# Kernel optimization log

Measured on AMD Instinct MI355X. Metric: run time of the kernel, lower is better.

## Reference

```python
import jax, jax.numpy as jnp
import numpy as np

NHEADS = 16
LORA_SCALE = 16.0 / 16.0  # alpha / r


def lora_linear(x, W, b, A, B):
    # base projection + low-rank LoRA path: x@W^T + b + s*(x@A^T)@B^T
    base = jnp.einsum('bse,oe->bso', x, W) + b
    low = jnp.einsum('bse,re->bsr', x, A)  # [B,S,r]
    return base + LORA_SCALE * jnp.einsum('bsr,or->bso', low, B)


def setup_inputs() -> dict:
    key = jax.random.key(0)
    E, R = 1024, 16
    ks = jax.random.split(key, 20)
    d = {'x': jax.random.normal(ks[0], (4, 1024, E), jnp.float32)}
    i = 1
    for p in ('q', 'k', 'v', 'o'):
        d[f'{p}_w'] = jax.random.normal(ks[i], (E, E), jnp.float32) * 0.02; i += 1
        d[f'{p}_b'] = jax.random.normal(ks[i], (E,), jnp.float32) * 0.02; i += 1
        d[f'{p}_la'] = jax.random.normal(ks[i], (R, E), jnp.float32) * 0.02; i += 1
        d[f'{p}_lb'] = jax.random.normal(ks[i], (E, R), jnp.float32) * 0.02; i += 1
    return d


def reference(x, q_w, q_b, q_la, q_lb, k_w, k_b, k_la, k_lb,
              v_w, v_b, v_la, v_lb, o_w, o_b, o_la, o_lb):
    B, S, E = x.shape
    H = NHEADS
    D = E // H
    q = lora_linear(x, q_w, q_b, q_la, q_lb).reshape(B, S, H, D)
    k = lora_linear(x, k_w, k_b, k_la, k_lb).reshape(B, S, H, D)
    v = lora_linear(x, v_w, v_b, v_la, v_lb).reshape(B, S, H, D)
    scores = jnp.einsum('bshd,bthd->bhst', q, k) / jnp.sqrt(jnp.asarray(D, x.dtype))
    attn = jax.nn.softmax(scores, axis=-1)
    ctx = jnp.einsum('bhst,bthd->bshd', attn, v).reshape(B, S, E)
    return lora_linear(ctx, o_w, o_b, o_la, o_lb)
```

## Files before the change

kernel.cpp:

```cpp
#include <hip/hip_runtime.h>
#include <cstdint>


typedef __attribute__((ext_vector_type(8))) short bf16x8;
typedef __attribute__((ext_vector_type(4))) float f32x4;
typedef __attribute__((ext_vector_type(16))) float f32x16;
typedef __attribute__((ext_vector_type(4))) unsigned short u16x4;
typedef __attribute__((ext_vector_type(4))) unsigned int u32x4;

__device__ __forceinline__ short f2bf(float f) {
  unsigned u = __builtin_bit_cast(unsigned, f);
  u += 0x7FFFu + ((u >> 16) & 1u);
  return (short)(u >> 16);
}

typedef __attribute__((address_space(1))) const unsigned int as1_uint;
typedef __attribute__((address_space(3))) unsigned int as3_uint;

__device__ __forceinline__ void gload_lds16(const short* g, const short* l) {
  __builtin_amdgcn_global_load_lds((as1_uint*)g,
      (as3_uint*)(unsigned int)(uintptr_t)l, 16, 0, 0);
}

__device__ __forceinline__ unsigned cvtpk(float lo, float hi) {
  unsigned r;
  asm("v_cvt_pk_bf16_f32 %0, %1, %2" : "=v"(r) : "v"(lo), "v"(hi));
  return r;
}
__device__ __forceinline__ void plswap(unsigned &a, unsigned &b) {
  asm("v_permlane32_swap_b32 %0, %1" : "+v"(a), "+v"(b));
}

__device__ __forceinline__ void build_pfrag(const f32x16 &s, bf16x8 &f0, bf16x8 &f1) {
  unsigned x0 = cvtpk(s[0], s[1]),  x1 = cvtpk(s[2], s[3]);
  unsigned x2 = cvtpk(s[4], s[5]),  x3 = cvtpk(s[6], s[7]);
  plswap(x0, x2); plswap(x1, x3);
  unsigned y0 = cvtpk(s[8], s[9]),  y1 = cvtpk(s[10], s[11]);
  unsigned y2 = cvtpk(s[12], s[13]), y3 = cvtpk(s[14], s[15]);
  plswap(y0, y2); plswap(y1, y3);
  u32x4 a = {x0, x1, x2, x3}, b = {y0, y1, y2, y3};
  f0 = __builtin_bit_cast(bf16x8, a);
  f1 = __builtin_bit_cast(bf16x8, b);
}

__global__ void build_x(const float* __restrict__ x, short* __restrict__ xb) {
  int idx = blockIdx.x * 256 + threadIdx.x;
  f32x4 v = ((const f32x4*)x)[idx];
  u16x4 o;
  o[0] = (unsigned short)f2bf(v[0]);
  o[1] = (unsigned short)f2bf(v[1]);
  o[2] = (unsigned short)f2bf(v[2]);
  o[3] = (unsigned short)f2bf(v[3]);
  ((u16x4*)xb)[idx] = o;
}

__global__ void fold_w(const float* __restrict__ wq, const float* __restrict__ wk,
                       const float* __restrict__ wv, const float* __restrict__ wo,
                       const float* __restrict__ bq, const float* __restrict__ bk,
                       const float* __restrict__ bv, const float* __restrict__ bo,
                       const float* __restrict__ aq, const float* __restrict__ ak,
                       const float* __restrict__ av, const float* __restrict__ ao,
                       short* __restrict__ out) {
  const int p = blockIdx.y;
  const float* W  = (p == 0) ? wq : (p == 1) ? wk : (p == 2) ? wv : wo;
  const float* Bm = (p == 0) ? bq : (p == 1) ? bk : (p == 2) ? bv : bo;
  const float* A  = (p == 0) ? aq : (p == 1) ? ak : (p == 2) ? av : ao;
  const int idx = blockIdx.x * 256 + threadIdx.x;
  const int n = idx >> 8;
  const int e4 = idx & 255;
  f32x4 acc = ((const f32x4*)(W + (size_t)n * 1024))[e4];
  const float* br = Bm + n * 16;
  #pragma unroll
  for (int r = 0; r < 16; ++r) {
    const f32x4 a4 = ((const f32x4*)(A + (size_t)r * 1024))[e4];
    const float b = br[r];
    acc[0] += b * a4[0];
    acc[1] += b * a4[1];
    acc[2] += b * a4[2];
    acc[3] += b * a4[3];
  }
  u16x4 o;
  o[0] = (unsigned short)f2bf(acc[0]);
  o[1] = (unsigned short)f2bf(acc[1]);
  o[2] = (unsigned short)f2bf(acc[2]);
  o[3] = (unsigned short)f2bf(acc[3]);
  *(u16x4*)(out + (size_t)p * 1048576 + (size_t)idx * 4) = o;
}

__device__ __forceinline__ void gemm_core_p3(const short* __restrict__ xrow,
                                             const short* __restrict__ wrow,
                                             short (&As)[3][8192], short (&Bs)[3][8192],
                                             f32x4 (&acc)[4][4]) {
  const int tid = threadIdx.x;
  const int wv = tid >> 6, lane = tid & 63;
  const int wr = wv >> 1, wc = wv & 1;
  const int lrow = lane & 15, lk = lane >> 4;
  const int srow = lane >> 3, sphys = lane & 7;

#define STAGE_G(buf, kt)                                                       \
  {                                                                            \
    _Pragma("unroll")                                                          \
    for (int i = 0; i < 4; ++i) {                                              \
      const int ch = i * 4 + wv;                                               \
      const int row = ch * 8 + srow;                                           \
      const int sl = sphys ^ (row & 7);                                        \
      gload_lds16(xrow + (size_t)row * 1024 + (kt) * 64 + sl * 8, As[buf] + ch * 512); \
      gload_lds16(wrow + (size_t)row * 1024 + (kt) * 64 + sl * 8, Bs[buf] + ch * 512); \
    }                                                                          \
  }

  STAGE_G(0, 0);
  STAGE_G(1, 1);
  int cur = 0;
  for (int kt = 0; kt < 16; ++kt) {
    if (kt < 14) {
      const int nb = (cur == 0) ? 2 : (cur - 1);
      STAGE_G(nb, kt + 2);
      asm volatile("s_waitcnt vmcnt(16)" ::: "memory");
    } else if (kt == 14) {
      asm volatile("s_waitcnt vmcnt(8)" ::: "memory");
    } else {
      asm volatile("s_waitcnt vmcnt(0)" ::: "memory");
    }
    __builtin_amdgcn_s_barrier();

    #pragma unroll
    for (int kc = 0; kc < 2; ++kc) {
      bf16x8 af[4], bw[4];
      #pragma unroll
      for (int mi = 0; mi < 4; ++mi) {
        const int row = wr * 64 + mi * 16 + lrow;
        const int slot = (kc * 4 + lk) ^ (row & 7);
        af[mi] = *(const bf16x8*)(As[cur] + row * 64 + slot * 8);
      }
      #pragma unroll
      for (int nj = 0; nj < 4; ++nj) {
        const int row = wc * 64 + nj * 16 + lrow;
        const int slot = (kc * 4 + lk) ^ (row & 7);
        bw[nj] = *(const bf16x8*)(Bs[cur] + row * 64 + slot * 8);
      }
      #pragma unroll
      for (int mi = 0; mi < 4; ++mi)
        #pragma unroll
        for (int nj = 0; nj < 4; ++nj)
          acc[mi][nj] = __builtin_amdgcn_mfma_f32_16x16x32_bf16(af[mi], bw[nj], acc[mi][nj], 0, 0, 0);
    }

    asm volatile("s_waitcnt lgkmcnt(0)" ::: "memory");
    __builtin_amdgcn_s_barrier();
    cur = (cur == 2) ? 0 : (cur + 1);
  }
#undef STAGE_G
}

__global__ __launch_bounds__(256)
void gemm_qkv(const short* __restrict__ xb, const short* __restrict__ wb,
              const float* __restrict__ biasq, const float* __restrict__ biask,
              const float* __restrict__ biasv,
              short* __restrict__ qbuf, short* __restrict__ kbuf, short* __restrict__ vtb) {
  __shared__ short As[3][8192];
  __shared__ short Bs[3][8192];
  const int wg = blockIdx.x;
  const int xcd = wg & 7, ix = wg >> 3;
  const int bcol = xcd * 3 + ix % 3;
  const int brow = ix / 3;
  const int p = bcol >> 3;

  const f32x4 fz = {0.f, 0.f, 0.f, 0.f};
  f32x4 acc[4][4];
  #pragma unroll
  for (int a = 0; a < 4; ++a)
    #pragma unroll
    for (int b = 0; b < 4; ++b) acc[a][b] = fz;

  gemm_core_p3(xb + (size_t)brow * 128 * 1024,
               wb + (size_t)bcol * 128 * 1024, As, Bs, acc);

  const int tid = threadIdx.x;
  const int wv = tid >> 6, lane = tid & 63;
  const int wr = wv >> 1, wc = wv & 1;
  const int lrow = lane & 15, lk = lane >> 4;
  const float* bias = (p == 0) ? biasq : (p == 1) ? biask : biasv;
  const float oscale = (p == 0) ? 0.18033688f : 1.0f;
  const int c0 = (bcol & 7) * 128;
  float bcv[4];
  #pragma unroll
  for (int nj = 0; nj < 4; ++nj)
    bcv[nj] = bias[c0 + wc * 64 + nj * 16 + lrow];

  #pragma unroll
  for (int mi = 0; mi < 4; ++mi) {
    #pragma unroll
    for (int r = 0; r < 4; ++r) {
      const int gr = brow * 128 + wr * 64 + mi * 16 + lk * 4 + r;
      const int bb = gr >> 10, s = gr & 1023;
      #pragma unroll
      for (int nj = 0; nj < 4; ++nj) {
        const int gc = c0 + wc * 64 + nj * 16 + lrow;
        const float v = (acc[mi][nj][r] + bcv[nj]) * oscale;
        const int h = gc >> 6, d = gc & 63;
        const int bh = bb * 16 + h;
        if (p == 2)
          vtb[((size_t)bh * 64 + d) * 1024 + s] = f2bf(v);
        else
          ((p == 0) ? qbuf : kbuf)[((size_t)bh * 1024 + s) * 64 + d] = f2bf(v);
      }
    }
  }
}

__global__ __launch_bounds__(256)
void attn_kernel(const short* __restrict__ qbuf, const short* __restrict__ kbuf,
                 const short* __restrict__ vtb, short* __restrict__ cb) {
  __shared__ short Ks[2][64 * 64];
  __shared__ short Vs[2][64 * 64];
  const int bh = blockIdx.x, qt = blockIdx.y;
  const int tid = threadIdx.x, w = tid >> 6, lane = tid & 63;
  const int l31 = lane & 31, hi = lane >> 5;
  const int srow = lane >> 3, sphys = lane & 7;
  const short* Qp = qbuf + (size_t)bh * 65536;
  const short* Kp = kbuf + (size_t)bh * 65536;
  const short* Vp = vtb + (size_t)bh * 65536;
  const int q0 = qt * 128 + w * 32;

  bf16x8 bq[4];
  #pragma unroll
  for (int kc = 0; kc < 4; ++kc)
    bq[kc] = *(const bf16x8*)(Qp + (size_t)(q0 + l31) * 64 + kc * 16 + hi * 8);

  const f32x16 fz16 = {0.f,0.f,0.f,0.f,0.f,0.f,0.f,0.f,0.f,0.f,0.f,0.f,0.f,0.f,0.f,0.f};
  float m_run = -1e30f, l_run = 0.f;
  f32x16 acc0 = fz16, acc1 = fz16;

  #define STAGE_KV(buf, tt)                                                  \
    {                                                                        \
      const int t0s = (tt) * 64;                                             \
      _Pragma("unroll")                                                      \
      for (int i = 0; i < 2; ++i) {                                          \
        const int ch = i * 4 + w;                                            \
        const int row = ch * 8 + srow;                                       \
        const int sl = sphys ^ (row & 7);                                    \
        gload_lds16(Kp + (size_t)(t0s + row) * 64 + sl * 8, Ks[buf] + ch * 512); \
        gload_lds16(Vp + (size_t)row * 1024 + t0s + sl * 8, Vs[buf] + ch * 512); \
      }                                                                      \
    }

  STAGE_KV(0, 0);
  __syncthreads();

  int cur = 0;
  for (int tt = 0; tt < 16; ++tt) {
    if (tt < 15) STAGE_KV(cur ^ 1, tt + 1);

    f32x16 s0 = fz16, s1 = fz16;
    #pragma unroll
    for (int kc = 0; kc < 4; ++kc) {
      const int slot = (kc * 2 + hi) ^ (l31 & 7);
      const bf16x8 ak0 = *(const bf16x8*)(Ks[cur] + l31 * 64 + slot * 8);
      const bf16x8 ak1 = *(const bf16x8*)(Ks[cur] + (32 + l31) * 64 + slot * 8);
      s0 = __builtin_amdgcn_mfma_f32_32x32x16_bf16(ak0, bq[kc], s0, 0, 0, 0);
      s1 = __builtin_amdgcn_mfma_f32_32x32x16_bf16(ak1, bq[kc], s1, 0, 0, 0);
    }

    float tm = s0[0];
    #pragma unroll
    for (int r = 1; r < 16; ++r) tm = fmaxf(tm, s0[r]);
    #pragma unroll
    for (int r = 0; r < 16; ++r) tm = fmaxf(tm, s1[r]);
    tm = fmaxf(tm, __shfl_xor(tm, 32, 64));
    const float mn = fmaxf(m_run, tm);
    const float alpha = exp2f(m_run - mn);
    m_run = mn;
    float rs = 0.f;
    #pragma unroll
    for (int r = 0; r < 16; ++r) { const float p = exp2f(s0[r] - mn); s0[r] = p; rs += p; }
    #pragma unroll
    for (int r = 0; r < 16; ++r) { const float p = exp2f(s1[r] - mn); s1[r] = p; rs += p; }
    rs += __shfl_xor(rs, 32, 64);
    l_run = l_run * alpha + rs;
    #pragma unroll
    for (int r = 0; r < 16; ++r) { acc0[r] *= alpha; acc1[r] *= alpha; }

    bf16x8 pf[4];
    build_pfrag(s0, pf[0], pf[1]);
    build_pfrag(s1, pf[2], pf[3]);

    #pragma unroll
    for (int kc4 = 0; kc4 < 4; ++kc4) {
      const int slot = (kc4 * 2 + hi) ^ (l31 & 7);
      const bf16x8 av0 = *(const bf16x8*)(Vs[cur] + l31 * 64 + slot * 8);
      const bf16x8 av1 = *(const bf16x8*)(Vs[cur] + (32 + l31) * 64 + slot * 8);
      acc0 = __builtin_amdgcn_mfma_f32_32x32x16_bf16(av0, pf[kc4], acc0, 0, 0, 0);
      acc1 = __builtin_amdgcn_mfma_f32_32x32x16_bf16(av1, pf[kc4], acc1, 0, 0, 0);
    }

    __syncthreads();
    cur ^= 1;
  }

  const int bb = bh >> 4, h = bh & 15;
  const int s = q0 + l31;
  short* crow = cb + (size_t)(bb * 1024 + s) * 1024 + h * 64;
  const float inv = 1.f / l_run;
  #pragma unroll
  for (int rp = 0; rp < 8; ++rp) {
    const int r = rp * 2;
    const int d = (r & 3) + 8 * (r >> 2) + 4 * hi;
    const unsigned p0 = (unsigned)(unsigned short)f2bf(acc0[r] * inv)
                      | ((unsigned)(unsigned short)f2bf(acc0[r + 1] * inv) << 16);
    const unsigned p1 = (unsigned)(unsigned short)f2bf(acc1[r] * inv)
                      | ((unsigned)(unsigned short)f2bf(acc1[r + 1] * inv) << 16);
    *(unsigned*)(crow + d) = p0;
    *(unsigned*)(crow + 32 + d) = p1;
  }
  #undef STAGE_KV
}

__global__ __launch_bounds__(256)
void gemm_o(const short* __restrict__ cb, const short* __restrict__ wo,
            const float* __restrict__ biaso, float* __restrict__ out) {
  __shared__ short As[3][8192];
  __shared__ short Bs[3][8192];
  const int brow = blockIdx.y, bcol = blockIdx.x;
  const f32x4 fz = {0.f, 0.f, 0.f, 0.f};
  f32x4 acc[4][4];
  #pragma unroll
  for (int a = 0; a < 4; ++a)
    #pragma unroll
    for (int b = 0; b < 4; ++b) acc[a][b] = fz;

  gemm_core_p3(cb + (size_t)brow * 128 * 1024, wo + (size_t)bcol * 128 * 1024,
               As, Bs, acc);

  const int tid = threadIdx.x;
  const int wv = tid >> 6, lane = tid & 63;
  const int wr = wv >> 1, wc = wv & 1;
  const int lrow = lane & 15, lk = lane >> 4;
  float bcv[4];
  #pragma unroll
  for (int nj = 0; nj < 4; ++nj)
    bcv[nj] = biaso[bcol * 128 + wc * 64 + nj * 16 + lrow];

  #pragma unroll
  for (int mi = 0; mi < 4; ++mi) {
    #pragma unroll
    for (int r = 0; r < 4; ++r) {
      const int gr = brow * 128 + wr * 64 + mi * 16 + lk * 4 + r;
      #pragma unroll
      for (int nj = 0; nj < 4; ++nj) {
        const int gc = bcol * 128 + wc * 64 + nj * 16 + lrow;
        out[(size_t)gr * 1024 + gc] = acc[mi][nj][r] + bcv[nj];
      }
    }
  }
}

extern "C" void kernel_launch(void* const* d_in, const int* in_sizes, int n_in,
                              void* d_out, int out_size, void* d_ws, size_t ws_size,
                              hipStream_t stream) {
  (void)in_sizes; (void)n_in; (void)out_size; (void)ws_size;
  const float* x   = (const float*)d_in[0];
  const float* qw  = (const float*)d_in[1];
  const float* qb  = (const float*)d_in[2];
  const float* qla = (const float*)d_in[3];
  const float* qlb = (const float*)d_in[4];
  const float* kw  = (const float*)d_in[5];
  const float* kb  = (const float*)d_in[6];
  const float* kla = (const float*)d_in[7];
  const float* klb = (const float*)d_in[8];
  const float* vw  = (const float*)d_in[9];
  const float* vb  = (const float*)d_in[10];
  const float* vla = (const float*)d_in[11];
  const float* vlb = (const float*)d_in[12];
  const float* ow  = (const float*)d_in[13];
  const float* ob  = (const float*)d_in[14];
  const float* ola = (const float*)d_in[15];
  const float* olb = (const float*)d_in[16];

  short* xb   = (short*)d_ws;
  short* wb   = xb + (size_t)4096 * 1024;
  short* qbuf = wb + (size_t)4 * 1024 * 1024;
  short* kbuf = qbuf + (size_t)4194304;
  short* vtb  = kbuf + (size_t)4194304;

  build_x<<<4096, 256, 0, stream>>>(x, xb);
  fold_w<<<dim3(1024, 4), 256, 0, stream>>>(qw, kw, vw, ow, qlb, klb, vlb, olb,
                                            qla, kla, vla, ola, wb);
  gemm_qkv<<<768, 256, 0, stream>>>(xb, wb, qb, kb, vb, qbuf, kbuf, vtb);
  attn_kernel<<<dim3(64, 8), 256, 0, stream>>>(qbuf, kbuf, vtb, xb);
  gemm_o<<<dim3(8, 32), 256, 0, stream>>>(xb, wb + (size_t)3 * 1024 * 1024, ob, (float*)d_out);
}
```

Baseline: 133.8 us.

## Merge prep kernels, double-buffer QKV GEMM, shrink attention blocks, lazy softmax rescale

After: 135.0 us. No clear change (+0.9%).

```diff
diff --git a/kernel.cpp b/kernel.cpp
--- a/kernel.cpp
+++ b/kernel.cpp
@@ -43,48 +43,287 @@
   f1 = __builtin_bit_cast(bf16x8, b);
 }
 
-__global__ void build_x(const float* __restrict__ x, short* __restrict__ xb) {
-  int idx = blockIdx.x * 256 + threadIdx.x;
-  f32x4 v = ((const f32x4*)x)[idx];
-  u16x4 o;
-  o[0] = (unsigned short)f2bf(v[0]);
-  o[1] = (unsigned short)f2bf(v[1]);
-  o[2] = (unsigned short)f2bf(v[2]);
-  o[3] = (unsigned short)f2bf(v[3]);
-  ((u16x4*)xb)[idx] = o;
-}
-
-__global__ void fold_w(const float* __restrict__ wq, const float* __restrict__ wk,
-                       const float* __restrict__ wv, const float* __restrict__ wo,
-                       const float* __restrict__ bq, const float* __restrict__ bk,
-                       const float* __restrict__ bv, const float* __restrict__ bo,
-                       const float* __restrict__ aq, const float* __restrict__ ak,
-                       const float* __restrict__ av, const float* __restrict__ ao,
-                       short* __restrict__ out) {
-  const int p = blockIdx.y;
-  const float* W  = (p == 0) ? wq : (p == 1) ? wk : (p == 2) ? wv : wo;
-  const float* Bm = (p == 0) ? bq : (p == 1) ? bk : (p == 2) ? bv : bo;
-  const float* A  = (p == 0) ? aq : (p == 1) ? ak : (p == 2) ? av : ao;
-  const int idx = blockIdx.x * 256 + threadIdx.x;
-  const int n = idx >> 8;
-  const int e4 = idx & 255;
-  f32x4 acc = ((const f32x4*)(W + (size_t)n * 1024))[e4];
-  const float* br = Bm + n * 16;
-  #pragma unroll
-  for (int r = 0; r < 16; ++r) {
-    const f32x4 a4 = ((const f32x4*)(A + (size_t)r * 1024))[e4];
-    const float b = br[r];
-    acc[0] += b * a4[0];
-    acc[1] += b * a4[1];
-    acc[2] += b * a4[2];
-    acc[3] += b * a4[3];
-  }
-  u16x4 o;
-  o[0] = (unsigned short)f2bf(acc[0]);
-  o[1] = (unsigned short)f2bf(acc[1]);
-  o[2] = (unsigned short)f2bf(acc[2]);
-  o[3] = (unsigned short)f2bf(acc[3]);
-  *(u16x4*)(out + (size_t)p * 1048576 + (size_t)idx * 4) = o;
+__global__ void prep_kernel(const float* __restrict__ x, short* __restrict__ xb,
+                            const float* __restrict__ wq, const float* __restrict__ wk,
+                            const float* __restrict__ wv, const float* __restrict__ wo,
+                            const float* __restrict__ bq, const float* __restrict__ bk,
+                            const float* __restrict__ bv, const float* __restrict__ bo,
+                            const float* __restrict__ aq, const float* __restrict__ ak,
+                            const float* __restrict__ av, const float* __restrict__ ao,
+                            short* __restrict__ wbo) {
+  const int b = blockIdx.x;
+  if (b < 4096) {
+    const int idx = b * 256 + threadIdx.x;
+    f32x4 v = ((const f32x4*)x)[idx];
+    u16x4 o;
+    o[0] = (unsigned short)f2bf(v[0]);
+    o[1] = (unsigned short)f2bf(v[1]);
+    o[2] = (unsigned short)f2bf(v[2]);
+    o[3] = (unsigned short)f2bf(v[3]);
+    ((u16x4*)xb)[idx] = o;
+  } else {
+    const int bb = b - 4096;
+    const int p = bb >> 10;
+    const float* W  = (p == 0) ? wq : (p == 1) ? wk : (p == 2) ? wv : wo;
+    const float* Bm = (p == 0) ? bq : (p == 1) ? bk : (p == 2) ? bv : bo;
+    const float* A  = (p == 0) ? aq : (p == 1) ? ak : (p == 2) ? av : ao;
+    const int idx = (bb & 1023) * 256 + threadIdx.x;
+    const int n = idx >> 8;
+    const int e4 = idx & 255;
+    f32x4 acc = ((const f32x4*)(W + (size_t)n * 1024))[e4];
+    const float* br = Bm + n * 16;
+    #pragma unroll
+    for (int r = 0; r < 16; ++r) {
+      const f32x4 a4 = ((const f32x4*)(A + (size_t)r * 1024))[e4];
+      const float bl = br[r];
+      acc[0] += bl * a4[0];
+      acc[1] += bl * a4[1];
+      acc[2] += bl * a4[2];
+      acc[3] += bl * a4[3];
+    }
+    u16x4 o;
+    o[0] = (unsigned short)f2bf(acc[0]);
+    o[1] = (unsigned short)f2bf(acc[1]);
+    o[2] = (unsigned short)f2bf(acc[2]);
+    o[3] = (unsigned short)f2bf(acc[3]);
+    *(u16x4*)(wbo + (size_t)p * 1048576 + (size_t)idx * 4) = o;
+  }
+}
+
+__device__ __forceinline__ void gemm_core_db(const short* __restrict__ xrow,
+                                             const short* __restrict__ wrow,
+                                             short (&As)[2][8192], short (&Bs)[2][8192],
+                                             f32x4 (&acc)[4][4]) {
+  const int tid = threadIdx.x;
+  const int wv = tid >> 6, lane = tid & 63;
+  const int wr = wv >> 1, wc = wv & 1;
+  const int lrow = lane & 15, lk = lane >> 4;
+  const int srow = lane >> 3, sphys = lane & 7;
+
+#define STAGE_G(buf, kt)                                                       \
+  {                                                                            \
+    _Pragma("unroll")                                                          \
+    for (int i = 0; i < 4; ++i) {                                              \
+      const int ch = i * 4 + wv;                                               \
+      const int row = ch * 8 + srow;                                           \
+      const int sl = sphys ^ (row & 7);                                        \
+      gload_lds16(xrow + (size_t)row * 1024 + (kt) * 64 + sl * 8, As[buf] + ch * 512); \
+      gload_lds16(wrow + (size_t)row * 1024 + (kt) * 64 + sl * 8, Bs[buf] + ch * 512); \
+    }                                                                          \
+  }
+
+  STAGE_G(0, 0);
+  __syncthreads();
+  int cur = 0;
+  for (int kt = 0; kt < 16; ++kt) {
+    if (kt < 15) STAGE_G(cur ^ 1, kt + 1);
+    #pragma unroll
+    for (int kc = 0; kc < 2; ++kc) {
+      bf16x8 af[4], bw[4];
+      #pragma unroll
+      for (int mi = 0; mi < 4; ++mi) {
+        const int row = wr * 64 + mi * 16 + lrow;
+        const int slot = (kc * 4 + lk) ^ (row & 7);
+        af[mi] = *(const bf16x8*)(As[cur] + row * 64 + slot * 8);
+      }
+      #pragma unroll
+      for (int nj = 0; nj < 4; ++nj) {
+        const int row = wc * 64 + nj * 16 + lrow;
+        const int slot = (kc * 4 + lk) ^ (row & 7);
+        bw[nj] = *(const bf16x8*)(Bs[cur] + row * 64 + slot * 8);
+      }
+      #pragma unroll
+      for (int mi = 0; mi < 4; ++mi)
+        #pragma unroll
+        for (int nj = 0; nj < 4; ++nj)
+          acc[mi][nj] = __builtin_amdgcn_mfma_f32_16x16x32_bf16(af[mi], bw[nj], acc[mi][nj], 0, 0, 0);
+    }
+    __syncthreads();
+    cur ^= 1;
+  }
+#undef STAGE_G
+}
+
+__global__ __launch_bounds__(256)
+void gemm_qkv(const short* __restrict__ xb, const short* __restrict__ wb,
+              const float* __restrict__ biasq, const float* __restrict__ biask,
+              const float* __restrict__ biasv,
+              short* __restrict__ qbuf, short* __restrict__ kbuf, short* __restrict__ vtb) {
+  __shared__ short As[2][8192];
+  __shared__ short Bs[2][8192];
+  const int wg = blockIdx.x;
+  const int xcd = wg & 7, ix = wg >> 3;
+  const int bcol = xcd * 3 + ix % 3;
+  const int brow = ix / 3;
+  const int p = bcol >> 3;
+
+  const f32x4 fz = {0.f, 0.f, 0.f, 0.f};
+  f32x4 acc[4][4];
+  #pragma unroll
+  for (int a = 0; a < 4; ++a)
+    #pragma unroll
+    for (int b = 0; b < 4; ++b) acc[a][b] = fz;
+
+  gemm_core_db(xb + (size_t)brow * 128 * 1024,
+               wb + (size_t)bcol * 128 * 1024, As, Bs, acc);
+
+  const int tid = threadIdx.x;
+  const int wv = tid >> 6, lane = tid & 63;
+  const int wr = wv >> 1, wc = wv & 1;
+  const int lrow = lane & 15, lk = lane >> 4;
+  const float* bias = (p == 0) ? biasq : (p == 1) ? biask : biasv;
+  const float oscale = (p == 0) ? 0.18033688f : 1.0f;
+  const int c0 = (bcol & 7) * 128;
+  float bcv[4];
+  #pragma unroll
+  for (int nj = 0; nj < 4; ++nj)
+    bcv[nj] = bias[c0 + wc * 64 + nj * 16 + lrow];
+
+  #pragma unroll
+  for (int mi = 0; mi < 4; ++mi) {
+    #pragma unroll
+    for (int r = 0; r < 4; ++r) {
+      const int gr = brow * 128 + wr * 64 + mi * 16 + lk * 4 + r;
+      const int bb = gr >> 10, s = gr & 1023;
+      #pragma unroll
+      for (int nj = 0; nj < 4; ++nj) {
+        const int gc = c0 + wc * 64 + nj * 16 + lrow;
+        const float v = (acc[mi][nj][r] + bcv[nj]) * oscale;
+        const int h = gc >> 6, d = gc & 63;
+        const int bh = bb * 16 + h;
+        if (p == 2)
+          vtb[((size_t)bh * 64 + d) * 1024 + s] = f2bf(v);
+        else
+          ((p == 0) ? qbuf : kbuf)[((size_t)bh * 1024 + s) * 64 + d] = f2bf(v);
+      }
+    }
+  }
+}
+
+__global__ __launch_bounds__(128)
+void attn_kernel(const short* __restrict__ qbuf, const short* __restrict__ kbuf,
+                 const short* __restrict__ vtb, short* __restrict__ cb) {
+  __shared__ short Ks[2][64 * 64];
+  __shared__ short Vs[2][64 * 64];
+  const int bh = blockIdx.x, qt = blockIdx.y;
+  const int tid = threadIdx.x, w = tid >> 6, lane = tid & 63;
+  const int l31 = lane & 31, hi = lane >> 5;
+  const int srow = lane >> 3, sphys = lane & 7;
+  const short* Qp = qbuf + (size_t)bh * 65536;
+  const short* Kp = kbuf + (size_t)bh * 65536;
+  const short* Vp = vtb + (size_t)bh * 65536;
+  const int q0 = qt * 64 + w * 32;
+
+  bf16x8 bq[4];
+  #pragma unroll
+  for (int kc = 0; kc < 4; ++kc)
+    bq[kc] = *(const bf16x8*)(Qp + (size_t)(q0 + l31) * 64 + kc * 16 + hi * 8);
+
+  const f32x16 fz16 = {0.f,0.f,0.f,0.f,0.f,0.f,0.f,0.f,0.f,0.f,0.f,0.f,0.f,0.f,0.f,0.f};
+  float m_run = -1e30f, l_run = 0.f;
+  f32x16 acc0 = fz16, acc1 = fz16;
+
+  #define STAGE_KV(buf, tt)                                                  \
+    {                                                                        \
+      const int t0s = (tt) * 64;                                             \
+      _Pragma("unroll")                                                      \
+      for (int i = 0; i < 4; ++i) {                                          \
+        const int ch = i * 2 + w;                                            \
+        const int row = ch * 8 + srow;                                       \
+        const int sl = sphys ^ (row & 7);                                    \
+        gload_lds16(Kp + (size_t)(t0s + row) * 64 + sl * 8, Ks[buf] + ch * 512); \
+        gload_lds16(Vp + (size_t)row * 1024 + t0s + sl * 8, Vs[buf] + ch * 512); \
+      }                                                                      \
+    }
+
+  STAGE_KV(0, 0);
+  __syncthreads();
+
+  int cur = 0;
+  for (int tt = 0; tt < 16; ++tt) {
+    if (tt < 15) STAGE_KV(cur ^ 1, tt + 1);
+
+    f32x16 s0 = fz16, s1 = fz16;
+    #pragma unroll
+    for (int kc = 0; kc < 4; ++kc) {
+      const int slot = (kc * 2 + hi) ^ (l31 & 7);
+      const bf16x8 ak0 = *(const bf16x8*)(Ks[cur] + l31 * 64 + slot * 8);
+      const bf16x8 ak1 = *(const bf16x8*)(Ks[cur] + (32 + l31) * 64 + slot * 8);
+      s0 = __builtin_amdgcn_mfma_f32_32x32x16_bf16(ak0, bq[kc], s0, 0, 0, 0);
+      s1 = __builtin_amdgcn_mfma_f32_32x32x16_bf16(ak1, bq[kc], s1, 0, 0, 0);
+    }
+
+    float t16[16];
+    #pragma unroll
+    for (int r = 0; r < 8; ++r) t16[r] = fmaxf(s0[2 * r], s0[2 * r + 1]);
+    #pragma unroll
+    for (int r = 0; r < 8; ++r) t16[8 + r] = fmaxf(s1[2 * r], s1[2 * r + 1]);
+    #pragma unroll
+    for (int r = 0; r < 8; ++r) t16[r] = fmaxf(t16[r], t16[r + 8]);
+    #pragma unroll
+    for (int r = 0; r < 4; ++r) t16[r] = fmaxf(t16[r], t16[r + 4]);
+    float tm = fmaxf(fmaxf(t16[0], t16[1]), fmaxf(t16[2], t16[3]));
+    tm = fmaxf(tm, __shfl_xor(tm, 32, 64));
+
+    if (__any(tm - m_run > 8.0f)) {
+      const float mn = fmaxf(m_run, tm);
+      const float alpha = exp2f(m_run - mn);
+      m_run = mn;
+      l_run *= alpha;
+      #pragma unroll
+      for (int r = 0; r < 16; ++r) { acc0[r] *= alpha; acc1[r] *= alpha; }
+    }
+
+    float a16[16];
+    #pragma unroll
+    for (int r = 0; r < 16; ++r) { s0[r] = exp2f(s0[r] - m_run); }
+    #pragma unroll
+    for (int r = 0; r < 16; ++r) { s1[r] = exp2f(s1[r] - m_run); }
+    #pragma unroll
+    for (int r = 0; r < 8; ++r) a16[r] = s0[2 * r] + s0[2 * r + 1];
+    #pragma unroll
+    for (int r = 0; r < 8; ++r) a16[8 + r] = s1[2 * r] + s1[2 * r + 1];
+    #pragma unroll
+    for (int r = 0; r < 8; ++r) a16[r] += a16[r + 8];
+    #pragma unroll
+    for (int r = 0; r < 4; ++r) a16[r] += a16[r + 4];
+    float rs = (a16[0] + a16[1]) + (a16[2] + a16[3]);
+    rs += __shfl_xor(rs, 32, 64);
+    l_run += rs;
+
+    bf16x8 pf[4];
+    build_pfrag(s0, pf[0], pf[1]);
+    build_pfrag(s1, pf[2], pf[3]);
+
+    #pragma unroll
+    for (int kc4 = 0; kc4 < 4; ++kc4) {
+      const int slot = (kc4 * 2 + hi) ^ (l31 & 7);
+      const bf16x8 av0 = *(const bf16x8*)(Vs[cur] + l31 * 64 + slot * 8);
+      const bf16x8 av1 = *(const bf16x8*)(Vs[cur] + (32 + l31) * 64 + slot * 8);
+      acc0 = __builtin_amdgcn_mfma_f32_32x32x16_bf16(av0, pf[kc4], acc0, 0, 0, 0);
+      acc1 = __builtin_amdgcn_mfma_f32_32x32x16_bf16(av1, pf[kc4], acc1, 0, 0, 0);
+    }
+
+    __syncthreads();
+    cur ^= 1;
+  }
+
+  const int bb = bh >> 4, h = bh & 15;
+  const int s = q0 + l31;
+  short* crow = cb + (size_t)(bb * 1024 + s) * 1024 + h * 64;
+  const float inv = 1.f / l_run;
+  #pragma unroll
+  for (int rp = 0; rp < 8; ++rp) {
+    const int r = rp * 2;
+    const int d = (r & 3) + 8 * (r >> 2) + 4 * hi;
+    const unsigned p0 = (unsigned)(unsigned short)f2bf(acc0[r] * inv)
+                      | ((unsigned)(unsigned short)f2bf(acc0[r + 1] * inv) << 16);
+    const unsigned p1 = (unsigned)(unsigned short)f2bf(acc1[r] * inv)
+                      | ((unsigned)(unsigned short)f2bf(acc1[r + 1] * inv) << 16);
+    *(unsigned*)(crow + d) = p0;
+    *(unsigned*)(crow + 32 + d) = p1;
+  }
+  #undef STAGE_KV
 }
 
 __device__ __forceinline__ void gemm_core_p3(const short* __restrict__ xrow,
@@ -151,169 +390,6 @@
     cur = (cur == 2) ? 0 : (cur + 1);
   }
 #undef STAGE_G
-}
-
-__global__ __launch_bounds__(256)
-void gemm_qkv(const short* __restrict__ xb, const short* __restrict__ wb,
-              const float* __restrict__ biasq, const float* __restrict__ biask,
-              const float* __restrict__ biasv,
-              short* __restrict__ qbuf, short* __restrict__ kbuf, short* __restrict__ vtb) {
-  __shared__ short As[3][8192];
-  __shared__ short Bs[3][8192];
-  const int wg = blockIdx.x;
-  const int xcd = wg & 7, ix = wg >> 3;
-  const int bcol = xcd * 3 + ix % 3;
-  const int brow = ix / 3;
-  const int p = bcol >> 3;
-
-  const f32x4 fz = {0.f, 0.f, 0.f, 0.f};
-  f32x4 acc[4][4];
-  #pragma unroll
-  for (int a = 0; a < 4; ++a)
-    #pragma unroll
-    for (int b = 0; b < 4; ++b) acc[a][b] = fz;
-
-  gemm_core_p3(xb + (size_t)brow * 128 * 1024,
-               wb + (size_t)bcol * 128 * 1024, As, Bs, acc);
-
-  const int tid = threadIdx.x;
-  const int wv = tid >> 6, lane = tid & 63;
-  const int wr = wv >> 1, wc = wv & 1;
-  const int lrow = lane & 15, lk = lane >> 4;
-  const float* bias = (p == 0) ? biasq : (p == 1) ? biask : biasv;
-  const float oscale = (p == 0) ? 0.18033688f : 1.0f;
-  const int c0 = (bcol & 7) * 128;
-  float bcv[4];
-  #pragma unroll
-  for (int nj = 0; nj < 4; ++nj)
-    bcv[nj] = bias[c0 + wc * 64 + nj * 16 + lrow];
-
-  #pragma unroll
-  for (int mi = 0; mi < 4; ++mi) {
-    #pragma unroll
-    for (int r = 0; r < 4; ++r) {
-      const int gr = brow * 128 + wr * 64 + mi * 16 + lk * 4 + r;
-      const int bb = gr >> 10, s = gr & 1023;
-      #pragma unroll
-      for (int nj = 0; nj < 4; ++nj) {
-        const int gc = c0 + wc * 64 + nj * 16 + lrow;
-        const float v = (acc[mi][nj][r] + bcv[nj]) * oscale;
-        const int h = gc >> 6, d = gc & 63;
-        const int bh = bb * 16 + h;
-        if (p == 2)
-          vtb[((size_t)bh * 64 + d) * 1024 + s] = f2bf(v);
-        else
-          ((p == 0) ? qbuf : kbuf)[((size_t)bh * 1024 + s) * 64 + d] = f2bf(v);
-      }
-    }
-  }
-}
-
-__global__ __launch_bounds__(256)
-void attn_kernel(const short* __restrict__ qbuf, const short* __restrict__ kbuf,
-                 const short* __restrict__ vtb, short* __restrict__ cb) {
-  __shared__ short Ks[2][64 * 64];
-  __shared__ short Vs[2][64 * 64];
-  const int bh = blockIdx.x, qt = blockIdx.y;
-  const int tid = threadIdx.x, w = tid >> 6, lane = tid & 63;
-  const int l31 = lane & 31, hi = lane >> 5;
-  const int srow = lane >> 3, sphys = lane & 7;
-  const short* Qp = qbuf + (size_t)bh * 65536;
-  const short* Kp = kbuf + (size_t)bh * 65536;
-  const short* Vp = vtb + (size_t)bh * 65536;
-  const int q0 = qt * 128 + w * 32;
-
-  bf16x8 bq[4];
-  #pragma unroll
-  for (int kc = 0; kc < 4; ++kc)
-    bq[kc] = *(const bf16x8*)(Qp + (size_t)(q0 + l31) * 64 + kc * 16 + hi * 8);
-
-  const f32x16 fz16 = {0.f,0.f,0.f,0.f,0.f,0.f,0.f,0.f,0.f,0.f,0.f,0.f,0.f,0.f,0.f,0.f};
-  float m_run = -1e30f, l_run = 0.f;
-  f32x16 acc0 = fz16, acc1 = fz16;
-
-  #define STAGE_KV(buf, tt)                                                  \
-    {                                                                        \
-      const int t0s = (tt) * 64;                                             \
-      _Pragma("unroll")                                                      \
-      for (int i = 0; i < 2; ++i) {                                          \
-        const int ch = i * 4 + w;                                            \
-        const int row = ch * 8 + srow;                                       \
-        const int sl = sphys ^ (row & 7);                                    \
-        gload_lds16(Kp + (size_t)(t0s + row) * 64 + sl * 8, Ks[buf] + ch * 512); \
-        gload_lds16(Vp + (size_t)row * 1024 + t0s + sl * 8, Vs[buf] + ch * 512); \
-      }                                                                      \
-    }
-
-  STAGE_KV(0, 0);
-  __syncthreads();
-
-  int cur = 0;
-  for (int tt = 0; tt < 16; ++tt) {
-    if (tt < 15) STAGE_KV(cur ^ 1, tt + 1);
-
-    f32x16 s0 = fz16, s1 = fz16;
-    #pragma unroll
-    for (int kc = 0; kc < 4; ++kc) {
-      const int slot = (kc * 2 + hi) ^ (l31 & 7);
-      const bf16x8 ak0 = *(const bf16x8*)(Ks[cur] + l31 * 64 + slot * 8);
-      const bf16x8 ak1 = *(const bf16x8*)(Ks[cur] + (32 + l31) * 64 + slot * 8);
-      s0 = __builtin_amdgcn_mfma_f32_32x32x16_bf16(ak0, bq[kc], s0, 0, 0, 0);
-      s1 = __builtin_amdgcn_mfma_f32_32x32x16_bf16(ak1, bq[kc], s1, 0, 0, 0);
-    }
-
-    float tm = s0[0];
-    #pragma unroll
-    for (int r = 1; r < 16; ++r) tm = fmaxf(tm, s0[r]);
-    #pragma unroll
-    for (int r = 0; r < 16; ++r) tm = fmaxf(tm, s1[r]);
-    tm = fmaxf(tm, __shfl_xor(tm, 32, 64));
-    const float mn = fmaxf(m_run, tm);
-    const float alpha = exp2f(m_run - mn);
-    m_run = mn;
-    float rs = 0.f;
-    #pragma unroll
-    for (int r = 0; r < 16; ++r) { const float p = exp2f(s0[r] - mn); s0[r] = p; rs += p; }
-    #pragma unroll
-    for (int r = 0; r < 16; ++r) { const float p = exp2f(s1[r] - mn); s1[r] = p; rs += p; }
-    rs += __shfl_xor(rs, 32, 64);
-    l_run = l_run * alpha + rs;
-    #pragma unroll
-    for (int r = 0; r < 16; ++r) { acc0[r] *= alpha; acc1[r] *= alpha; }
-
-    bf16x8 pf[4];
-    build_pfrag(s0, pf[0], pf[1]);
-    build_pfrag(s1, pf[2], pf[3]);
-
-    #pragma unroll
-    for (int kc4 = 0; kc4 < 4; ++kc4) {
-      const int slot = (kc4 * 2 + hi) ^ (l31 & 7);
-      const bf16x8 av0 = *(const bf16x8*)(Vs[cur] + l31 * 64 + slot * 8);
-      const bf16x8 av1 = *(const bf16x8*)(Vs[cur] + (32 + l31) * 64 + slot * 8);
-      acc0 = __builtin_amdgcn_mfma_f32_32x32x16_bf16(av0, pf[kc4], acc0, 0, 0, 0);
-      acc1 = __builtin_amdgcn_mfma_f32_32x32x16_bf16(av1, pf[kc4], acc1, 0, 0, 0);
-    }
-
-    __syncthreads();
-    cur ^= 1;
-  }
-
-  const int bb = bh >> 4, h = bh & 15;
-  const int s = q0 + l31;
-  short* crow = cb + (size_t)(bb * 1024 + s) * 1024 + h * 64;
-  const float inv = 1.f / l_run;
-  #pragma unroll
-  for (int rp = 0; rp < 8; ++rp) {
-    const int r = rp * 2;
-    const int d = (r & 3) + 8 * (r >> 2) + 4 * hi;
-    const unsigned p0 = (unsigned)(unsigned short)f2bf(acc0[r] * inv)
-                      | ((unsigned)(unsigned short)f2bf(acc0[r + 1] * inv) << 16);
-    const unsigned p1 = (unsigned)(unsigned short)f2bf(acc1[r] * inv)
-                      | ((unsigned)(unsigned short)f2bf(acc1[r + 1] * inv) << 16);
-    *(unsigned*)(crow + d) = p0;
-    *(unsigned*)(crow + 32 + d) = p1;
-  }
-  #undef STAGE_KV
 }
 
 __global__ __launch_bounds__(256)
@@ -383,10 +459,10 @@
   short* kbuf = qbuf + (size_t)4194304;
   short* vtb  = kbuf + (size_t)4194304;
 
-  build_x<<<4096, 256, 0, stream>>>(x, xb);
-  fold_w<<<dim3(1024, 4), 256, 0, stream>>>(qw, kw, vw, ow, qlb, klb, vlb, olb,
-                                            qla, kla, vla, ola, wb);
+  prep_kernel<<<8192, 256, 0, stream>>>(x, xb, qw, kw, vw, ow,
+                                        qlb, klb, vlb, olb,
+                                        qla, kla, vla, ola, wb);
   gemm_qkv<<<768, 256, 0, stream>>>(xb, wb, qb, kb, vb, qbuf, kbuf, vtb);
-  attn_kernel<<<dim3(64, 8), 256, 0, stream>>>(qbuf, kbuf, vtb, xb);
+  attn_kernel<<<dim3(64, 16), 128, 0, stream>>>(qbuf, kbuf, vtb, xb);
   gemm_o<<<dim3(8, 32), 256, 0, stream>>>(xb, wb + (size_t)3 * 1024 * 1024, ob, (float*)d_out);
 }
```
